# Kernel tuning notes

Measured on AMD Instinct MI355X. Metric: run time of the kernel, lower is better.

Reference implementation:

```python
import jax, jax.numpy as jnp
import numpy as np
from jax import lax

DN = ('NCH', 'OIH', 'NCH')

def conv1d(x, w, b, pad=0):
    y = lax.conv_general_dilated(x, w, window_strides=(1,), padding=[(pad, pad)], dimension_numbers=DN)
    return y + b[None, :, None]

def conv_transpose1d(x, w_torch, b):
    # torch ConvTranspose1d weight: [C_in, C_out, K]; equivalent to full conv with flipped kernel
    k = w_torch.shape[-1]
    w = jnp.flip(jnp.transpose(w_torch, (1, 0, 2)), axis=-1)  # [C_out, C_in, K]
    y = lax.conv_general_dilated(x, w, window_strides=(1,), padding=[(k - 1, k - 1)], dimension_numbers=DN)
    return y + b[None, :, None]

def converter(signal, w1, b1, w2, b2, wt, bt, w3, b3):
    h = jax.nn.relu(conv1d(signal, w1, b1))          # [B,10,n-2]
    h = jax.nn.relu(conv1d(h, w2, b2))               # [B,10,n-2]
    h = jax.nn.relu(conv_transpose1d(h, wt, bt))     # [B,10,n]
    h = jax.nn.sigmoid(conv1d(h, w3, b3))            # [B,2,n]
    return h

def setup_inputs() -> dict:
    key = jax.random.key(0)
    ks = jax.random.split(key, 12)
    B, C, n = 32, 128, 8192
    signal = jax.random.normal(ks[0], (B, C, n), dtype=jnp.float32)
    curr_diag = jax.random.uniform(ks[1], (B, n - 1), dtype=jnp.float32) + 0.5
    s = 0.1
    return {
        'signal': signal,
        'curr_diag': curr_diag,
        'index_diag': 1,
        'w1': jax.random.normal(ks[2], (10, C, 3), dtype=jnp.float32) * s,
        'b1': jax.random.normal(ks[3], (10,), dtype=jnp.float32) * s,
        'w2': jax.random.normal(ks[4], (10, 10, 1), dtype=jnp.float32) * s,
        'b2': jax.random.normal(ks[5], (10,), dtype=jnp.float32) * s,
        'wt': jax.random.normal(ks[6], (10, 10, 3), dtype=jnp.float32) * s,
        'bt': jax.random.normal(ks[7], (10,), dtype=jnp.float32) * s,
        'w3': jax.random.normal(ks[8], (2, 10, 1), dtype=jnp.float32) * s,
        'b3': jax.random.normal(ks[9], (2,), dtype=jnp.float32) * s,
        'const': jnp.float32(0.99),
    }

def reference(signal, curr_diag, index_diag, w1, b1, w2, b2, wt, bt, w3, b3, const):
    n = signal.shape[-1]
    lr = converter(signal, w1, b1, w2, b2, wt, bt, w3, b3)  # [B,2,n]
    left, right = lr[:, 0, :], lr[:, 1, :]
    # diag_len = n - index_diag; next diag has length diag_len - 1
    mass_in = curr_diag[:, 1:] * right[:, 1:n - index_diag]
    mass_in = mass_in + curr_diag[:, :-1] * left[:, index_diag:n - 1]
    mass_out = right[:, 0:n - index_diag - 1] + left[:, index_diag + 1:n]
    next_diag = const * mass_in / mass_out
    next_diag = jnp.log(next_diag)
    next_diag = next_diag - jnp.mean(next_diag)
    return next_diag
```

## Files before the change

### kernel.cpp

```cpp
#include <hip/hip_runtime.h>
#include <math.h>

#define B    32
#define CIN  128
#define NN   8192
#define N1   8190
#define CH   10
#define TILE 256

__global__ __launch_bounds__(256) void k1_conv12(
    const float* __restrict__ sig, const float* __restrict__ w1, const float* __restrict__ b1,
    const float* __restrict__ w2, const float* __restrict__ b2, float* __restrict__ h2out)
{
    const int p  = blockIdx.x * 256 + threadIdx.x;
    const int t2 = 2 * p;
    const int b  = blockIdx.y;
    if (t2 >= N1) return;

    float y0[CH], y1[CH];
#pragma unroll
    for (int o = 0; o < CH; ++o) { y0[o] = b1[o]; y1[o] = b1[o]; }

    const float* sp = sig + (size_t)b * CIN * NN + t2;

#pragma unroll 4
    for (int ci = 0; ci < CIN; ++ci) {
        const float* s = sp + (size_t)ci * NN;
        const float2 lo = *(const float2*)(s);
        const float2 hi = *(const float2*)(s + 2);
        const float* wp = w1 + ci * 3;
#pragma unroll
        for (int o = 0; o < CH; ++o) {
            const float w0 = wp[o * CIN * 3 + 0];
            const float w1v = wp[o * CIN * 3 + 1];
            const float w2v = wp[o * CIN * 3 + 2];
            y0[o] = fmaf(w0, lo.x, y0[o]);
            y0[o] = fmaf(w1v, lo.y, y0[o]);
            y0[o] = fmaf(w2v, hi.x, y0[o]);
            y1[o] = fmaf(w0, lo.y, y1[o]);
            y1[o] = fmaf(w1v, hi.x, y1[o]);
            y1[o] = fmaf(w2v, hi.y, y1[o]);
        }
    }

#pragma unroll
    for (int o = 0; o < CH; ++o) { y0[o] = fmaxf(y0[o], 0.f); y1[o] = fmaxf(y1[o], 0.f); }

#pragma unroll
    for (int o = 0; o < CH; ++o) {
        float a0 = b2[o], a1 = b2[o];
#pragma unroll
        for (int i = 0; i < CH; ++i) {
            const float w = w2[o * CH + i];
            a0 = fmaf(w, y0[i], a0);
            a1 = fmaf(w, y1[i], a1);
        }
        float2 st; st.x = fmaxf(a0, 0.f); st.y = fmaxf(a1, 0.f);
        *(float2*)(h2out + ((size_t)b * CH + o) * N1 + t2) = st;
    }
}

__global__ __launch_bounds__(256) void k2_fused(
    const float* __restrict__ h2, const float* __restrict__ cd,
    const float* __restrict__ wt, const float* __restrict__ bt,
    const float* __restrict__ w3, const float* __restrict__ b3,
    const float* __restrict__ cstp, float* __restrict__ outv, float* __restrict__ bsums)
{
    const int b  = blockIdx.y;
    const int t0 = blockIdx.x * TILE;

    __shared__ float lsh[TILE + 4];
    __shared__ float rsh[TILE + 4];

    for (int s = t0 + threadIdx.x; s <= t0 + TILE + 2; s += 256) {
        if (s < NN) {
            float acc[CH];
#pragma unroll
            for (int o = 0; o < CH; ++o) acc[o] = bt[o];
#pragma unroll
            for (int i = 0; i < CH; ++i) {
                const float* hp = h2 + ((size_t)b * CH + i) * N1;
                const float v0 = (s < N1)            ? hp[s]     : 0.f;
                const float v1 = (s >= 1 && s <= N1) ? hp[s - 1] : 0.f;
                const float v2 = (s >= 2)            ? hp[s - 2] : 0.f;
                const float* wp = wt + (i * CH) * 3;
#pragma unroll
                for (int o = 0; o < CH; ++o) {
                    acc[o] = fmaf(wp[o * 3 + 0], v0, acc[o]);
                    acc[o] = fmaf(wp[o * 3 + 1], v1, acc[o]);
                    acc[o] = fmaf(wp[o * 3 + 2], v2, acc[o]);
                }
            }
            float l = b3[0], r = b3[1];
#pragma unroll
            for (int o = 0; o < CH; ++o) {
                const float h3 = fmaxf(acc[o], 0.f);
                l = fmaf(w3[o],      h3, l);
                r = fmaf(w3[CH + o], h3, r);
            }
            lsh[s - t0] = 1.f / (1.f + expf(-l));
            rsh[s - t0] = 1.f / (1.f + expf(-r));
        }
    }
    __syncthreads();

    const int t = t0 + threadIdx.x;
    float v = 0.f;
    if (t < N1) {
        const float c0 = cd[(size_t)b * (NN - 1) + t];
        const float c1 = cd[(size_t)b * (NN - 1) + t + 1];
        const float mi = c1 * rsh[threadIdx.x + 1] + c0 * lsh[threadIdx.x + 1];
        const float mo = rsh[threadIdx.x] + lsh[threadIdx.x + 2];
        v = logf(cstp[0] * mi / mo);
        outv[(size_t)b * N1 + t] = v;
    }

    __shared__ float red[256];
    red[threadIdx.x] = v;
    __syncthreads();
#pragma unroll
    for (int s = 128; s > 0; s >>= 1) {
        if (threadIdx.x < s) red[threadIdx.x] += red[threadIdx.x + s];
        __syncthreads();
    }
    if (threadIdx.x == 0) bsums[blockIdx.y * gridDim.x + blockIdx.x] = red[0];
}

__global__ __launch_bounds__(256) void k3_mean(const float* __restrict__ bsums, float* __restrict__ meanp)
{
    __shared__ float red[256];
    float s = 0.f;
    for (int i = threadIdx.x; i < 1024; i += 256) s += bsums[i];
    red[threadIdx.x] = s;
    __syncthreads();
#pragma unroll
    for (int st = 128; st > 0; st >>= 1) {
        if (threadIdx.x < st) red[threadIdx.x] += red[threadIdx.x + st];
        __syncthreads();
    }
    if (threadIdx.x == 0) meanp[0] = red[0] / (float)(B * N1);
}

__global__ __launch_bounds__(256) void k4_sub(float* __restrict__ outv, const float* __restrict__ meanp, int n)
{
    const int i = blockIdx.x * 256 + threadIdx.x;
    if (i < n) outv[i] -= meanp[0];
}

extern "C" void kernel_launch(void* const* d_in, const int* in_sizes, int n_in,
                              void* d_out, int out_size, void* d_ws, size_t ws_size,
                              hipStream_t stream)
{
    const float* sig = (const float*)d_in[0];
    const float* cd  = (const float*)d_in[1];
    const float* w1  = (const float*)d_in[3];
    const float* b1  = (const float*)d_in[4];
    const float* w2  = (const float*)d_in[5];
    const float* b2  = (const float*)d_in[6];
    const float* wt  = (const float*)d_in[7];
    const float* bt  = (const float*)d_in[8];
    const float* w3  = (const float*)d_in[9];
    const float* b3  = (const float*)d_in[10];
    const float* cst = (const float*)d_in[11];

    float* outv = (float*)d_out;

    float* ws   = (float*)d_ws;
    float* h2   = ws;
    float* bsum = h2 + (size_t)B * CH * N1;
    float* mean = bsum + 1024;

    dim3 blk(256);
    dim3 g1((N1 / 2 + 255) / 256, B);
    dim3 g2((N1 + TILE - 1) / TILE, B);

    k1_conv12<<<g1, blk, 0, stream>>>(sig, w1, b1, w2, b2, h2);
    k2_fused <<<g2, blk, 0, stream>>>(h2, cd, wt, bt, w3, b3, cst, outv, bsum);
    k3_mean  <<<dim3(1), blk, 0, stream>>>(bsum, mean);
    k4_sub   <<<dim3((out_size + 255) / 256), blk, 0, stream>>>(outv, mean, out_size);
}
```

Before: 270.2 us.

## Stage conv1 inputs through LDS chunks with register prefetch and transposed weights

```diff
diff --git a/kernel.cpp b/kernel.cpp
--- a/kernel.cpp
+++ b/kernel.cpp
@@ -1,129 +1,192 @@
 #include <hip/hip_runtime.h>
 #include <math.h>
 
-#define B    32
-#define CIN  128
-#define NN   8192
-#define N1   8190
-#define CH   10
-#define TILE 256
-
-__global__ __launch_bounds__(256) void k1_conv12(
-    const float* __restrict__ sig, const float* __restrict__ w1, const float* __restrict__ b1,
+#define B     32
+#define CIN   128
+#define NN    8192
+#define N1    8190
+#define N1P   8192
+#define CH    10
+#define CHUNK 16
+#define ROWF  260
+#define ROWF2 268
+
+__global__ void k0_prep(const float* __restrict__ w1, float* __restrict__ wT)
+{
+    const int i = blockIdx.x * 256 + threadIdx.x;
+    if (i < CIN * 32) {
+        const int ci = i >> 5, r = i & 31;
+        float v = 0.f;
+        if (r < 30) {
+            const int o = r / 3, k = r - o * 3;
+            v = w1[(o * CIN + ci) * 3 + k];
+        }
+        wT[i] = v;
+    }
+}
+
+__global__ __launch_bounds__(256, 4) void k1_conv12(
+    const float* __restrict__ sig, const float* __restrict__ wT, const float* __restrict__ b1,
     const float* __restrict__ w2, const float* __restrict__ b2, float* __restrict__ h2out)
 {
-    const int p  = blockIdx.x * 256 + threadIdx.x;
-    const int t2 = 2 * p;
-    const int b  = blockIdx.y;
-    if (t2 >= N1) return;
-
-    float y0[CH], y1[CH];
-#pragma unroll
-    for (int o = 0; o < CH; ++o) { y0[o] = b1[o]; y1[o] = b1[o]; }
-
-    const float* sp = sig + (size_t)b * CIN * NN + t2;
-
-#pragma unroll 4
-    for (int ci = 0; ci < CIN; ++ci) {
-        const float* s = sp + (size_t)ci * NN;
-        const float2 lo = *(const float2*)(s);
-        const float2 hi = *(const float2*)(s + 2);
-        const float* wp = w1 + ci * 3;
+    __shared__ float ls[CHUNK * ROWF];
+    const int tid = threadIdx.x;
+    const int b   = blockIdx.y;
+    const int t0  = blockIdx.x * 256;
+    const float* sb = sig + (size_t)b * CIN * NN;
+
+    float4 pf[5];
+
+    auto fetch = [&](int c) {
+#pragma unroll
+        for (int k = 0; k < 5; ++k) {
+            const int li = tid + k * 256;
+            if (k == 4 && tid >= 16) break;
+            const int row = li / 65, col = li - row * 65;
+            const int g = t0 + col * 4;
+            const float* p = sb + (size_t)(c * CHUNK + row) * NN + g;
+            float4 v = {0.f, 0.f, 0.f, 0.f};
+            if (g + 3 < NN) v = *(const float4*)p;
+            else {
+                if (g + 0 < NN) v.x = p[0];
+                if (g + 1 < NN) v.y = p[1];
+                if (g + 2 < NN) v.z = p[2];
+            }
+            pf[k] = v;
+        }
+    };
+    auto store_lds = [&]() {
+#pragma unroll
+        for (int k = 0; k < 5; ++k) {
+            const int li = tid + k * 256;
+            if (k == 4 && tid >= 16) break;
+            const int row = li / 65, col = li - row * 65;
+            *(float4*)&ls[row * ROWF + col * 4] = pf[k];
+        }
+    };
+
+    float y[CH];
+#pragma unroll
+    for (int o = 0; o < CH; ++o) y[o] = b1[o];
+
+    fetch(0);
+    for (int c = 0; c < CIN / CHUNK; ++c) {
+        __syncthreads();
+        store_lds();
+        __syncthreads();
+        if (c < CIN / CHUNK - 1) fetch(c + 1);
+
+        const float* wbase = wT + c * CHUNK * 32;
+#pragma unroll
+        for (int cl = 0; cl < CHUNK; ++cl) {
+            const float s0 = ls[cl * ROWF + tid + 0];
+            const float s1 = ls[cl * ROWF + tid + 1];
+            const float s2 = ls[cl * ROWF + tid + 2];
+            const float* wrow = wbase + cl * 32;
+#pragma unroll
+            for (int o = 0; o < CH; ++o) {
+                y[o] = fmaf(wrow[o * 3 + 0], s0, y[o]);
+                y[o] = fmaf(wrow[o * 3 + 1], s1, y[o]);
+                y[o] = fmaf(wrow[o * 3 + 2], s2, y[o]);
+            }
+        }
+    }
+
+    const int t = t0 + tid;
+    if (t < N1) {
+#pragma unroll
+        for (int o = 0; o < CH; ++o) y[o] = fmaxf(y[o], 0.f);
 #pragma unroll
         for (int o = 0; o < CH; ++o) {
-            const float w0 = wp[o * CIN * 3 + 0];
-            const float w1v = wp[o * CIN * 3 + 1];
-            const float w2v = wp[o * CIN * 3 + 2];
-            y0[o] = fmaf(w0, lo.x, y0[o]);
-            y0[o] = fmaf(w1v, lo.y, y0[o]);
-            y0[o] = fmaf(w2v, hi.x, y0[o]);
-            y1[o] = fmaf(w0, lo.y, y1[o]);
-            y1[o] = fmaf(w1v, hi.x, y1[o]);
-            y1[o] = fmaf(w2v, hi.y, y1[o]);
-        }
-    }
-
-#pragma unroll
-    for (int o = 0; o < CH; ++o) { y0[o] = fmaxf(y0[o], 0.f); y1[o] = fmaxf(y1[o], 0.f); }
-
-#pragma unroll
-    for (int o = 0; o < CH; ++o) {
-        float a0 = b2[o], a1 = b2[o];
-#pragma unroll
-        for (int i = 0; i < CH; ++i) {
-            const float w = w2[o * CH + i];
-            a0 = fmaf(w, y0[i], a0);
-            a1 = fmaf(w, y1[i], a1);
-        }
-        float2 st; st.x = fmaxf(a0, 0.f); st.y = fmaxf(a1, 0.f);
-        *(float2*)(h2out + ((size_t)b * CH + o) * N1 + t2) = st;
-    }
-}
-
-__global__ __launch_bounds__(256) void k2_fused(
+            float a = b2[o];
+#pragma unroll
+            for (int i = 0; i < CH; ++i) a = fmaf(w2[o * CH + i], y[i], a);
+            h2out[((size_t)b * CH + o) * N1P + t] = fmaxf(a, 0.f);
+        }
+    }
+}
+
+__global__ __launch_bounds__(256, 4) void k2_fused(
     const float* __restrict__ h2, const float* __restrict__ cd,
     const float* __restrict__ wt, const float* __restrict__ bt,
     const float* __restrict__ w3, const float* __restrict__ b3,
     const float* __restrict__ cstp, float* __restrict__ outv, float* __restrict__ bsums)
 {
-    const int b  = blockIdx.y;
-    const int t0 = blockIdx.x * TILE;
-
-    __shared__ float lsh[TILE + 4];
-    __shared__ float rsh[TILE + 4];
-
-    for (int s = t0 + threadIdx.x; s <= t0 + TILE + 2; s += 256) {
-        if (s < NN) {
-            float acc[CH];
-#pragma unroll
-            for (int o = 0; o < CH; ++o) acc[o] = bt[o];
-#pragma unroll
-            for (int i = 0; i < CH; ++i) {
-                const float* hp = h2 + ((size_t)b * CH + i) * N1;
-                const float v0 = (s < N1)            ? hp[s]     : 0.f;
-                const float v1 = (s >= 1 && s <= N1) ? hp[s - 1] : 0.f;
-                const float v2 = (s >= 2)            ? hp[s - 2] : 0.f;
-                const float* wp = wt + (i * CH) * 3;
-#pragma unroll
-                for (int o = 0; o < CH; ++o) {
-                    acc[o] = fmaf(wp[o * 3 + 0], v0, acc[o]);
-                    acc[o] = fmaf(wp[o * 3 + 1], v1, acc[o]);
-                    acc[o] = fmaf(wp[o * 3 + 2], v2, acc[o]);
-                }
+    __shared__ float hs[CH * ROWF2];
+    __shared__ float lsh[260], rsh[260];
+    __shared__ float red[256];
+    const int tid = threadIdx.x;
+    const int b   = blockIdx.y;
+    const int t0  = blockIdx.x * 256;
+    const float* hb = h2 + (size_t)b * CH * N1P;
+
+    for (int li = tid; li < 660; li += 256) {
+        const int row = li / 66, col = li - row * 66;
+        const int g = t0 - 4 + col * 4;
+        const float* p = hb + (size_t)row * N1P + g;
+        float4 v = {0.f, 0.f, 0.f, 0.f};
+        if (g >= 0 && g + 3 < N1) v = *(const float4*)p;
+        else {
+            if (g + 0 >= 0 && g + 0 < N1) v.x = p[0];
+            if (g + 1 >= 0 && g + 1 < N1) v.y = p[1];
+            if (g + 2 >= 0 && g + 2 < N1) v.z = p[2];
+            if (g + 3 >= 0 && g + 3 < N1) v.w = p[3];
+        }
+        *(float4*)&hs[row * ROWF2 + col * 4] = v;
+    }
+    __syncthreads();
+
+    auto computeLR = [&](int sidx) {
+        float acc[CH];
+#pragma unroll
+        for (int o = 0; o < CH; ++o) acc[o] = bt[o];
+#pragma unroll
+        for (int i = 0; i < CH; ++i) {
+            const float a2 = hs[i * ROWF2 + sidx + 2];
+            const float a3 = hs[i * ROWF2 + sidx + 3];
+            const float a4 = hs[i * ROWF2 + sidx + 4];
+            const float* wp = wt + i * CH * 3;
+#pragma unroll
+            for (int o = 0; o < CH; ++o) {
+                acc[o] = fmaf(wp[o * 3 + 0], a4, acc[o]);
+                acc[o] = fmaf(wp[o * 3 + 1], a3, acc[o]);
+                acc[o] = fmaf(wp[o * 3 + 2], a2, acc[o]);
             }
-            float l = b3[0], r = b3[1];
-#pragma unroll
-            for (int o = 0; o < CH; ++o) {
-                const float h3 = fmaxf(acc[o], 0.f);
-                l = fmaf(w3[o],      h3, l);
-                r = fmaf(w3[CH + o], h3, r);
-            }
-            lsh[s - t0] = 1.f / (1.f + expf(-l));
-            rsh[s - t0] = 1.f / (1.f + expf(-r));
-        }
-    }
-    __syncthreads();
-
-    const int t = t0 + threadIdx.x;
+        }
+        float l = b3[0], r = b3[1];
+#pragma unroll
+        for (int o = 0; o < CH; ++o) {
+            const float h3 = fmaxf(acc[o], 0.f);
+            l = fmaf(w3[o],      h3, l);
+            r = fmaf(w3[CH + o], h3, r);
+        }
+        lsh[sidx] = 1.f / (1.f + __expf(-l));
+        rsh[sidx] = 1.f / (1.f + __expf(-r));
+    };
+
+    computeLR(tid);
+    if (tid < 3) computeLR(256 + tid);
+    __syncthreads();
+
+    const int t = t0 + tid;
     float v = 0.f;
     if (t < N1) {
         const float c0 = cd[(size_t)b * (NN - 1) + t];
         const float c1 = cd[(size_t)b * (NN - 1) + t + 1];
-        const float mi = c1 * rsh[threadIdx.x + 1] + c0 * lsh[threadIdx.x + 1];
-        const float mo = rsh[threadIdx.x] + lsh[threadIdx.x + 2];
-        v = logf(cstp[0] * mi / mo);
+        const float mi = c1 * rsh[tid + 1] + c0 * lsh[tid + 1];
+        const float mo = rsh[tid] + lsh[tid + 2];
+        v = __logf(cstp[0] * mi / mo);
         outv[(size_t)b * N1 + t] = v;
     }
 
-    __shared__ float red[256];
-    red[threadIdx.x] = v;
+    red[tid] = v;
     __syncthreads();
 #pragma unroll
     for (int s = 128; s > 0; s >>= 1) {
-        if (threadIdx.x < s) red[threadIdx.x] += red[threadIdx.x + s];
-        __syncthreads();
-    }
-    if (threadIdx.x == 0) bsums[blockIdx.y * gridDim.x + blockIdx.x] = red[0];
+        if (tid < s) red[tid] += red[tid + s];
+        __syncthreads();
+    }
+    if (tid == 0) bsums[blockIdx.y * gridDim.x + blockIdx.x] = red[0];
 }
 
 __global__ __launch_bounds__(256) void k3_mean(const float* __restrict__ bsums, float* __restrict__ meanp)
@@ -166,16 +229,17 @@
     float* outv = (float*)d_out;
 
     float* ws   = (float*)d_ws;
-    float* h2   = ws;
-    float* bsum = h2 + (size_t)B * CH * N1;
+    float* wT   = ws;
+    float* h2   = wT + CIN * 32;
+    float* bsum = h2 + (size_t)B * CH * N1P;
     float* mean = bsum + 1024;
 
     dim3 blk(256);
-    dim3 g1((N1 / 2 + 255) / 256, B);
-    dim3 g2((N1 + TILE - 1) / TILE, B);
-
-    k1_conv12<<<g1, blk, 0, stream>>>(sig, w1, b1, w2, b2, h2);
-    k2_fused <<<g2, blk, 0, stream>>>(h2, cd, wt, bt, w3, b3, cst, outv, bsum);
+    dim3 g1(32, B);
+
+    k0_prep  <<<dim3(16), blk, 0, stream>>>(w1, wT);
+    k1_conv12<<<g1, blk, 0, stream>>>(sig, wT, b1, w2, b2, h2);
+    k2_fused <<<g1, blk, 0, stream>>>(h2, cd, wt, bt, w3, b3, cst, outv, bsum);
     k3_mean  <<<dim3(1), blk, 0, stream>>>(bsum, mean);
     k4_sub   <<<dim3((out_size + 255) / 256), blk, 0, stream>>>(outv, mean, out_size);
 }
```

Result: faster. 255.2 us (-5.6%).
